# Performance work log

Measured on AMD Instinct MI355X. Metric: run time of the kernel, lower is better.

The kernel has to match this reference:

```python
import jax, jax.numpy as jnp
import numpy as np

WS = 4      # window_size
H = 128     # hidden_size
IN = 3      # input_size (1 control + 2 state channels)
OUT = 2     # out_size = input_size - 1


def _lstm_layer(x, Wih, Whh, b):
    # x: [B, S, Din] -> ys: [B, S, H], h/c: [B, H]. PyTorch gate order i,f,g,o.
    B = x.shape[0]
    xg = jnp.einsum('bsd,gd->bsg', x, Wih) + b  # precompute input projections

    def step(carry, xt):
        h, c = carry
        g = xt + h @ Whh.T
        i, f, gg, o = jnp.split(g, 4, axis=-1)
        c = jax.nn.sigmoid(f) * c + jax.nn.sigmoid(i) * jnp.tanh(gg)
        h = jax.nn.sigmoid(o) * jnp.tanh(c)
        return (h, c), h

    z = jnp.zeros((B, Whh.shape[1]), x.dtype)
    (h, c), ys = jax.lax.scan(step, (z, z), xg.transpose(1, 0, 2))
    return ys.transpose(1, 0, 2), h, c


def _lstm2(x, p):
    (Wih0, Whh0, b0), (Wih1, Whh1, b1) = p
    y0, h0, c0 = _lstm_layer(x, Wih0, Whh0, b0)
    y1, h1, c1 = _lstm_layer(y0, Wih1, Whh1, b1)
    return y1, jnp.stack([h0, h1]), jnp.stack([c0, c1])


def _forward(traj, Wih0, Whh0, bih0, bhh0, Wih1, Whh1, bih1, bhh1, Wl, bl):
    p = ((Wih0, Whh0, bih0 + bhh0), (Wih1, Whh1, bih1 + bhh1))
    head = lambda ys: ys[:, -1] @ Wl.T + bl  # linear applied to last LSTM step (== pred[:, -1])
    T = traj.shape[1]

    # initial window on raw trajectory
    ys, h, c = _lstm2(traj[:, :WS], p)
    out = traj[:, WS - 1:WS, 1:] + head(ys)[:, None, :]  # [B, 1, OUT]

    # warm-up phase: windows mix raw traj rows with predicted rows (features ordered [ctrl, out])
    for t in range(1, WS):
        tmp = jnp.concatenate([traj[:, WS + t:WS + t + 1, 0:1], out[:, t - 1:t, :]], axis=2)
        seq = jnp.concatenate([traj[:, t:WS + t - 1, :], tmp], axis=1)  # [B, WS, IN]
        ys, h, c = _lstm2(seq, p)
        out = jnp.concatenate([out, traj[:, WS + t - 1:WS + t, 1:] + head(ys)[:, None, :]], axis=1)

    nsteps = T - 2 * WS
    idx = WS + np.arange(nsteps)[:, None] + np.arange(WS)[None, :]  # [nsteps, WS]
    ctrl = traj[:, :, 0][:, idx].transpose(1, 0, 2)[..., None]      # [nsteps, B, WS, 1]

    def step(carry, ctrl_t):
        win, _, _ = carry
        seq = jnp.concatenate([win, ctrl_t], axis=2)  # [B, WS, OUT+1]
        ys, h, c = _lstm2(seq, p)
        new = win[:, -1, :] + head(ys)                # [B, OUT]
        win = jnp.concatenate([win[:, 1:], new[:, None, :]], axis=1)
        return (win, h, c), new

    (win, h, c), news = jax.lax.scan(step, (out, h, c), ctrl)
    out = jnp.concatenate([out, news.transpose(1, 0, 2)], axis=1)  # [B, T-WS, OUT]
    return out, h, c


def setup_inputs():
    key = jax.random.key(0)
    ks = jax.random.split(key, 11)
    B, T = 128, 256
    s = 1.0 / np.sqrt(H)
    u = lambda k, shp: jax.random.uniform(k, shp, jnp.float32, -s, s)
    return dict(
        one_full_traj=jax.random.normal(ks[0], (B, T, IN), jnp.float32),
        Wih0=u(ks[1], (4 * H, IN)), Whh0=u(ks[2], (4 * H, H)),
        bih0=u(ks[3], (4 * H,)), bhh0=u(ks[4], (4 * H,)),
        Wih1=u(ks[5], (4 * H, H)), Whh1=u(ks[6], (4 * H, H)),
        bih1=u(ks[7], (4 * H,)), bhh1=u(ks[8], (4 * H,)),
        Wl=u(ks[9], (OUT, H)), bl=u(ks[10], (OUT,)),
    )


def reference(one_full_traj, Wih0, Whh0, bih0, bhh0, Wih1, Whh1, bih1, bhh1, Wl, bl):
    # returns (out, h_n, c_n) matching torch's (out, hidden)
    return _forward(one_full_traj, Wih0, Whh0, bih0, bhh0, Wih1, Whh1, bih1, bhh1, Wl, bl)
```

## Files before the change

kernel.cpp:

```cpp
#include <hip/hip_runtime.h>

typedef _Float16 half2_t __attribute__((ext_vector_type(2)));
typedef unsigned int u32;

#define NW 252

__device__ inline u32 pk(float x, float y) {
  half2_t h; h.x = (_Float16)x; h.y = (_Float16)y;
  return __builtin_bit_cast(u32, h);
}

__device__ inline float fdot2(u32 a, u32 b, float c) {
#if __has_builtin(__builtin_amdgcn_fdot2)
  return __builtin_amdgcn_fdot2(__builtin_bit_cast(half2_t, a),
                                __builtin_bit_cast(half2_t, b), c, false);
#else
  half2_t ah = __builtin_bit_cast(half2_t, a);
  half2_t bh = __builtin_bit_cast(half2_t, b);
  return c + (float)ah.x * (float)bh.x + (float)ah.y * (float)bh.y;
#endif
}

__device__ inline float fast_rcp(float x) {
#if __has_builtin(__builtin_amdgcn_rcpf)
  return __builtin_amdgcn_rcpf(x);
#else
  return 1.0f / x;
#endif
}

__device__ inline float sigf(float x)  { return fast_rcp(1.0f + __expf(-x)); }
__device__ inline float tanh_(float x) { return 1.0f - 2.0f * fast_rcp(__expf(2.0f * x) + 1.0f); }

__device__ inline float quad_reduce(float v) {
  int x = __builtin_bit_cast(int, v);
  int y = __builtin_amdgcn_update_dpp(0, x, 0xB1, 0xF, 0xF, true);
  v += __builtin_bit_cast(float, y);
  x = __builtin_bit_cast(int, v);
  y = __builtin_amdgcn_update_dpp(0, x, 0x4E, 0xF, 0xF, true);
  v += __builtin_bit_cast(float, y);
  return v;
}

#define LOAD_SLICE(dst, basehalf)                                          \
  { const uint4* _p = (const uint4*)(basehalf) + ks * 4;                   \
    uint4 _q0 = _p[0], _q1 = _p[1], _q2 = _p[2], _q3 = _p[3];              \
    dst[0]=_q0.x;  dst[1]=_q0.y;  dst[2]=_q0.z;  dst[3]=_q0.w;             \
    dst[4]=_q1.x;  dst[5]=_q1.y;  dst[6]=_q1.z;  dst[7]=_q1.w;             \
    dst[8]=_q2.x;  dst[9]=_q2.y;  dst[10]=_q2.z; dst[11]=_q2.w;            \
    dst[12]=_q3.x; dst[13]=_q3.y; dst[14]=_q3.z; dst[15]=_q3.w; }

__global__ __launch_bounds__(512)
__attribute__((amdgpu_waves_per_eu(1, 2)))
void lstm_roll(
    const float* __restrict__ traj,
    const float* __restrict__ Wih0, const float* __restrict__ Whh0,
    const float* __restrict__ bih0, const float* __restrict__ bhh0,
    const float* __restrict__ Wih1, const float* __restrict__ Whh1,
    const float* __restrict__ bih1, const float* __restrict__ bhh1,
    const float* __restrict__ Wl,   const float* __restrict__ bl,
    float* __restrict__ out)
{
  const int b   = blockIdx.x;
  const int B   = gridDim.x;
  const int tid = threadIdx.x;
  const int j   = tid >> 2;
  const int ks  = tid & 3;

  __shared__ __align__(16) _Float16 h0buf[2][128];
  __shared__ __align__(16) _Float16 h1buf[2][128];
  __shared__ float sh_h1f[128];
  __shared__ float sh_Wl[256];
  __shared__ float trajS[256 * 3];
  __shared__ float preds[NW * 2];
  __shared__ __align__(16) float sh_w0b0[128 * 20];
  __shared__ __align__(16) float sh_b1[128 * 4];

  for (int i = tid; i < 768; i += 512) trajS[i] = traj[b * 768 + i];
  if (tid < 256) sh_Wl[tid] = Wl[tid];
  float blv = 0.0f;
  if (tid < 8) blv = bl[tid >> 2];
  {
    const int jj = tid >> 2, g = tid & 3;
    const int row = g * 128 + jj;
    sh_w0b0[jj * 20 + g * 4 + 0] = Wih0[row * 3 + 0];
    sh_w0b0[jj * 20 + g * 4 + 1] = Wih0[row * 3 + 1];
    sh_w0b0[jj * 20 + g * 4 + 2] = Wih0[row * 3 + 2];
    sh_w0b0[jj * 20 + g * 4 + 3] = bih0[row] + bhh0[row];
    sh_b1[jj * 4 + g] = bih1[row] + bhh1[row];
  }

  u32 wA[64], wB[64], wC[64];
#pragma unroll
  for (int g = 0; g < 4; ++g) {
    const int row = g * 128 + j;
    const float4* pA = (const float4*)(Whh0 + row * 128 + ks * 32);
    const float4* pB = (const float4*)(Wih1 + row * 128 + ks * 32);
    const float4* pC = (const float4*)(Whh1 + row * 128 + ks * 32);
#pragma unroll
    for (int q = 0; q < 8; ++q) {
      float4 fa = pA[q], fb = pB[q], fc = pC[q];
      wA[g*16 + q*2    ] = pk(fa.x, fa.y);
      wA[g*16 + q*2 + 1] = pk(fa.z, fa.w);
      wB[g*16 + q*2    ] = pk(fb.x, fb.y);
      wB[g*16 + q*2 + 1] = pk(fb.z, fb.w);
      wC[g*16 + q*2    ] = pk(fc.x, fc.y);
      wC[g*16 + q*2 + 1] = pk(fc.z, fc.w);
    }
  }

  float c0 = 0.f, c1 = 0.f, h0f = 0.f, h1f = 0.f;

  auto L0STEP = [&](int w_, int t_, int p_) {
    float acc0 = 0.f, acc1 = 0.f, acc2 = 0.f, acc3 = 0.f;
    if (ks == 0) {
      float x0, x1, x2;
      if (w_ < 4) {
        if (w_ == 0 || t_ < 3) {
          const float* r = &trajS[(w_ + t_) * 3];
          x0 = r[0]; x1 = r[1]; x2 = r[2];
        } else {
          x0 = trajS[(4 + w_) * 3];
          x1 = preds[(w_ - 1) * 2];
          x2 = preds[(w_ - 1) * 2 + 1];
        }
      } else {
        const int s_ = w_ - 4;
        x0 = preds[(s_ + t_) * 2];
        x1 = preds[(s_ + t_) * 2 + 1];
        x2 = trajS[(w_ + t_) * 3];
      }
      const float4* wb = (const float4*)&sh_w0b0[j * 20];
      float4 q0 = wb[0], q1 = wb[1], q2 = wb[2], q3 = wb[3];
      acc0 = q0.w + q0.x * x0 + q0.y * x1 + q0.z * x2;
      acc1 = q1.w + q1.x * x0 + q1.y * x1 + q1.z * x2;
      acc2 = q2.w + q2.x * x0 + q2.y * x1 + q2.z * x2;
      acc3 = q3.w + q3.x * x0 + q3.y * x1 + q3.z * x2;
    }
    if (t_ > 0) {
      u32 su[16];
      LOAD_SLICE(su, h0buf[p_]);
#pragma unroll
      for (int kk = 0; kk < 16; ++kk) {
        acc0 = fdot2(wA[     kk], su[kk], acc0);
        acc1 = fdot2(wA[16 + kk], su[kk], acc1);
        acc2 = fdot2(wA[32 + kk], su[kk], acc2);
        acc3 = fdot2(wA[48 + kk], su[kk], acc3);
      }
    }
    acc0 = quad_reduce(acc0); acc1 = quad_reduce(acc1);
    acc2 = quad_reduce(acc2); acc3 = quad_reduce(acc3);
    float ig = sigf(acc0), fg = sigf(acc1), gg = tanh_(acc2), og = sigf(acc3);
    float cp = t_ ? c0 : 0.f;
    c0  = fg * cp + ig * gg;
    h0f = og * tanh_(c0);
    if (ks == 0) h0buf[p_ ^ 1][j] = (_Float16)h0f;
  };

  auto L1STEP = [&](int t_, int p_) {
    float acc0 = 0.f, acc1 = 0.f, acc2 = 0.f, acc3 = 0.f;
    if (ks == 0) {
      float4 bb = *(const float4*)&sh_b1[j * 4];
      acc0 = bb.x; acc1 = bb.y; acc2 = bb.z; acc3 = bb.w;
    }
    {
      u32 sy[16];
      LOAD_SLICE(sy, h0buf[p_]);
#pragma unroll
      for (int kk = 0; kk < 16; ++kk) {
        acc0 = fdot2(wB[     kk], sy[kk], acc0);
        acc1 = fdot2(wB[16 + kk], sy[kk], acc1);
        acc2 = fdot2(wB[32 + kk], sy[kk], acc2);
        acc3 = fdot2(wB[48 + kk], sy[kk], acc3);
      }
    }
    if (t_ > 0) {
      u32 sh[16];
      LOAD_SLICE(sh, h1buf[p_]);
#pragma unroll
      for (int kk = 0; kk < 16; ++kk) {
        acc0 = fdot2(wC[     kk], sh[kk], acc0);
        acc1 = fdot2(wC[16 + kk], sh[kk], acc1);
        acc2 = fdot2(wC[32 + kk], sh[kk], acc2);
        acc3 = fdot2(wC[48 + kk], sh[kk], acc3);
      }
    }
    acc0 = quad_reduce(acc0); acc1 = quad_reduce(acc1);
    acc2 = quad_reduce(acc2); acc3 = quad_reduce(acc3);
    float ig = sigf(acc0), fg = sigf(acc1), gg = tanh_(acc2), og = sigf(acc3);
    float cp = t_ ? c1 : 0.f;
    c1  = fg * cp + ig * gg;
    h1f = og * tanh_(c1);
    if (ks == 0) {
      h1buf[p_ ^ 1][j] = (_Float16)h1f;
      if (t_ == 3) sh_h1f[j] = h1f;
    }
  };

  auto HD = [&](int w_) {
    if (tid < 8) {
      const int d = tid >> 2;
      const float* wrow = &sh_Wl[d * 128 + ks * 32];
      const float* hrow = &sh_h1f[ks * 32];
      float s = 0.f;
#pragma unroll
      for (int m = 0; m < 32; ++m) s = fmaf(wrow[m], hrow[m], s);
      s = quad_reduce(s);
      if (ks == 0) {
        float base = (w_ < 4) ? trajS[(3 + w_) * 3 + 1 + d] : preds[(w_ - 1) * 2 + d];
        preds[w_ * 2 + d] = base + s + blv;
      }
    }
  };

  __syncthreads();

  int p = 0;
  L0STEP(0, 0, p);
  __syncthreads(); p ^= 1;

#pragma unroll 1
  for (int w = 0; w < NW; ++w) {
    if (w > 0) HD(w - 1);
    L0STEP(w, 1, p);
    L1STEP(0, p);
    __syncthreads(); p ^= 1;
    L0STEP(w, 2, p);
    L1STEP(1, p);
    __syncthreads(); p ^= 1;
    L0STEP(w, 3, p);
    L1STEP(2, p);
    __syncthreads(); p ^= 1;
    L1STEP(3, p);
    if (w < NW - 1) L0STEP(w + 1, 0, p);
    __syncthreads(); p ^= 1;
  }

  HD(NW - 1);
  __syncthreads();

  for (int i = tid; i < NW * 2; i += 512) out[b * (NW * 2) + i] = preds[i];
  if (ks == 0) {
    const int oh = B * NW * 2;
    const int oc = oh + 2 * B * 128;
    out[oh +            b * 128 + j] = h0f;
    out[oh + B * 128 +  b * 128 + j] = h1f;
    out[oc +            b * 128 + j] = c0;
    out[oc + B * 128 +  b * 128 + j] = c1;
  }
}

extern "C" void kernel_launch(void* const* d_in, const int* in_sizes, int n_in,
                              void* d_out, int out_size, void* d_ws, size_t ws_size,
                              hipStream_t stream) {
  const float* traj = (const float*)d_in[0];
  const float* Wih0 = (const float*)d_in[1];
  const float* Whh0 = (const float*)d_in[2];
  const float* bih0 = (const float*)d_in[3];
  const float* bhh0 = (const float*)d_in[4];
  const float* Wih1 = (const float*)d_in[5];
  const float* Whh1 = (const float*)d_in[6];
  const float* bih1 = (const float*)d_in[7];
  const float* bhh1 = (const float*)d_in[8];
  const float* Wl   = (const float*)d_in[9];
  const float* bl   = (const float*)d_in[10];

  const int B = in_sizes[0] / (256 * 3);
  hipLaunchKernelGGL(lstm_roll, dim3(B), dim3(512), 0, stream,
                     traj, Wih0, Whh0, bih0, bhh0, Wih1, Whh1, bih1, bhh1,
                     Wl, bl, (float*)d_out);
}
```

Baseline: 1.379 ms.

## Split each hidden unit's dot products across 8 threads with 1024-thread blocks

Doubles the block to 1024 threads so each hidden unit is handled by 8 lanes instead of 4. Each lane keeps half as many packed fp16 weights in registers and does half the dot-product work per step. The partial sums are combined with a quad DPP reduce plus one xor shuffle. This shortens the serial per-step latency of the recurrent matvec, at the cost of an extra cross-lane reduction step, more waves contending at each barrier, and redundant gate math on the extra lanes.

```diff
diff --git a/kernel.cpp b/kernel.cpp
--- a/kernel.cpp
+++ b/kernel.cpp
@@ -41,17 +41,13 @@
   v += __builtin_bit_cast(float, y);
   return v;
 }
-
-#define LOAD_SLICE(dst, basehalf)                                          \
-  { const uint4* _p = (const uint4*)(basehalf) + ks * 4;                   \
-    uint4 _q0 = _p[0], _q1 = _p[1], _q2 = _p[2], _q3 = _p[3];              \
-    dst[0]=_q0.x;  dst[1]=_q0.y;  dst[2]=_q0.z;  dst[3]=_q0.w;             \
-    dst[4]=_q1.x;  dst[5]=_q1.y;  dst[6]=_q1.z;  dst[7]=_q1.w;             \
-    dst[8]=_q2.x;  dst[9]=_q2.y;  dst[10]=_q2.z; dst[11]=_q2.w;            \
-    dst[12]=_q3.x; dst[13]=_q3.y; dst[14]=_q3.z; dst[15]=_q3.w; }
-
-__global__ __launch_bounds__(512)
-__attribute__((amdgpu_waves_per_eu(1, 2)))
+__device__ inline float red8(float v) {
+  v = quad_reduce(v);
+  v += __shfl_xor(v, 4);
+  return v;
+}
+
+__global__ __launch_bounds__(1024)
 void lstm_roll(
     const float* __restrict__ traj,
     const float* __restrict__ Wih0, const float* __restrict__ Whh0,
@@ -64,8 +60,8 @@
   const int b   = blockIdx.x;
   const int B   = gridDim.x;
   const int tid = threadIdx.x;
-  const int j   = tid >> 2;
-  const int ks  = tid & 3;
+  const int j   = tid >> 3;
+  const int ks  = tid & 7;
 
   __shared__ __align__(16) _Float16 h0buf[2][128];
   __shared__ __align__(16) _Float16 h1buf[2][128];
@@ -76,11 +72,11 @@
   __shared__ __align__(16) float sh_w0b0[128 * 20];
   __shared__ __align__(16) float sh_b1[128 * 4];
 
-  for (int i = tid; i < 768; i += 512) trajS[i] = traj[b * 768 + i];
+  for (int i = tid; i < 768; i += 1024) trajS[i] = traj[b * 768 + i];
   if (tid < 256) sh_Wl[tid] = Wl[tid];
   float blv = 0.0f;
   if (tid < 8) blv = bl[tid >> 2];
-  {
+  if (tid < 512) {
     const int jj = tid >> 2, g = tid & 3;
     const int row = g * 128 + jj;
     sh_w0b0[jj * 20 + g * 4 + 0] = Wih0[row * 3 + 0];
@@ -90,22 +86,22 @@
     sh_b1[jj * 4 + g] = bih1[row] + bhh1[row];
   }
 
-  u32 wA[64], wB[64], wC[64];
+  u32 wA[32], wB[32], wC[32];
 #pragma unroll
   for (int g = 0; g < 4; ++g) {
     const int row = g * 128 + j;
-    const float4* pA = (const float4*)(Whh0 + row * 128 + ks * 32);
-    const float4* pB = (const float4*)(Wih1 + row * 128 + ks * 32);
-    const float4* pC = (const float4*)(Whh1 + row * 128 + ks * 32);
-#pragma unroll
-    for (int q = 0; q < 8; ++q) {
+    const float4* pA = (const float4*)(Whh0 + row * 128 + ks * 16);
+    const float4* pB = (const float4*)(Wih1 + row * 128 + ks * 16);
+    const float4* pC = (const float4*)(Whh1 + row * 128 + ks * 16);
+#pragma unroll
+    for (int q = 0; q < 4; ++q) {
       float4 fa = pA[q], fb = pB[q], fc = pC[q];
-      wA[g*16 + q*2    ] = pk(fa.x, fa.y);
-      wA[g*16 + q*2 + 1] = pk(fa.z, fa.w);
-      wB[g*16 + q*2    ] = pk(fb.x, fb.y);
-      wB[g*16 + q*2 + 1] = pk(fb.z, fb.w);
-      wC[g*16 + q*2    ] = pk(fc.x, fc.y);
-      wC[g*16 + q*2 + 1] = pk(fc.z, fc.w);
+      wA[g*8 + q*2    ] = pk(fa.x, fa.y);
+      wA[g*8 + q*2 + 1] = pk(fa.z, fa.w);
+      wB[g*8 + q*2    ] = pk(fb.x, fb.y);
+      wB[g*8 + q*2 + 1] = pk(fb.z, fb.w);
+      wC[g*8 + q*2    ] = pk(fc.x, fc.y);
+      wC[g*8 + q*2 + 1] = pk(fc.z, fc.w);
     }
   }
 
@@ -138,18 +134,19 @@
       acc3 = q3.w + q3.x * x0 + q3.y * x1 + q3.z * x2;
     }
     if (t_ > 0) {
-      u32 su[16];
-      LOAD_SLICE(su, h0buf[p_]);
-#pragma unroll
-      for (int kk = 0; kk < 16; ++kk) {
-        acc0 = fdot2(wA[     kk], su[kk], acc0);
-        acc1 = fdot2(wA[16 + kk], su[kk], acc1);
-        acc2 = fdot2(wA[32 + kk], su[kk], acc2);
-        acc3 = fdot2(wA[48 + kk], su[kk], acc3);
-      }
-    }
-    acc0 = quad_reduce(acc0); acc1 = quad_reduce(acc1);
-    acc2 = quad_reduce(acc2); acc3 = quad_reduce(acc3);
+      const uint4* _p = (const uint4*)(h0buf[p_]) + ks * 2;
+      uint4 q0 = _p[0], q1 = _p[1];
+      u32 s[8] = {q0.x, q0.y, q0.z, q0.w, q1.x, q1.y, q1.z, q1.w};
+#pragma unroll
+      for (int kk = 0; kk < 8; ++kk) {
+        acc0 = fdot2(wA[     kk], s[kk], acc0);
+        acc1 = fdot2(wA[ 8 + kk], s[kk], acc1);
+        acc2 = fdot2(wA[16 + kk], s[kk], acc2);
+        acc3 = fdot2(wA[24 + kk], s[kk], acc3);
+      }
+    }
+    acc0 = red8(acc0); acc1 = red8(acc1);
+    acc2 = red8(acc2); acc3 = red8(acc3);
     float ig = sigf(acc0), fg = sigf(acc1), gg = tanh_(acc2), og = sigf(acc3);
     float cp = t_ ? c0 : 0.f;
     c0  = fg * cp + ig * gg;
@@ -164,29 +161,31 @@
       acc0 = bb.x; acc1 = bb.y; acc2 = bb.z; acc3 = bb.w;
     }
     {
-      u32 sy[16];
-      LOAD_SLICE(sy, h0buf[p_]);
-#pragma unroll
-      for (int kk = 0; kk < 16; ++kk) {
-        acc0 = fdot2(wB[     kk], sy[kk], acc0);
-        acc1 = fdot2(wB[16 + kk], sy[kk], acc1);
-        acc2 = fdot2(wB[32 + kk], sy[kk], acc2);
-        acc3 = fdot2(wB[48 + kk], sy[kk], acc3);
+      const uint4* _p = (const uint4*)(h0buf[p_]) + ks * 2;
+      uint4 q0 = _p[0], q1 = _p[1];
+      u32 s[8] = {q0.x, q0.y, q0.z, q0.w, q1.x, q1.y, q1.z, q1.w};
+#pragma unroll
+      for (int kk = 0; kk < 8; ++kk) {
+        acc0 = fdot2(wB[     kk], s[kk], acc0);
+        acc1 = fdot2(wB[ 8 + kk], s[kk], acc1);
+        acc2 = fdot2(wB[16 + kk], s[kk], acc2);
+        acc3 = fdot2(wB[24 + kk], s[kk], acc3);
       }
     }
     if (t_ > 0) {
-      u32 sh[16];
-      LOAD_SLICE(sh, h1buf[p_]);
-#pragma unroll
-      for (int kk = 0; kk < 16; ++kk) {
-        acc0 = fdot2(wC[     kk], sh[kk], acc0);
-        acc1 = fdot2(wC[16 + kk], sh[kk], acc1);
-        acc2 = fdot2(wC[32 + kk], sh[kk], acc2);
-        acc3 = fdot2(wC[48 + kk], sh[kk], acc3);
-      }
-    }
-    acc0 = quad_reduce(acc0); acc1 = quad_reduce(acc1);
-    acc2 = quad_reduce(acc2); acc3 = quad_reduce(acc3);
+      const uint4* _p = (const uint4*)(h1buf[p_]) + ks * 2;
+      uint4 q0 = _p[0], q1 = _p[1];
+      u32 s[8] = {q0.x, q0.y, q0.z, q0.w, q1.x, q1.y, q1.z, q1.w};
+#pragma unroll
+      for (int kk = 0; kk < 8; ++kk) {
+        acc0 = fdot2(wC[     kk], s[kk], acc0);
+        acc1 = fdot2(wC[ 8 + kk], s[kk], acc1);
+        acc2 = fdot2(wC[16 + kk], s[kk], acc2);
+        acc3 = fdot2(wC[24 + kk], s[kk], acc3);
+      }
+    }
+    acc0 = red8(acc0); acc1 = red8(acc1);
+    acc2 = red8(acc2); acc3 = red8(acc3);
     float ig = sigf(acc0), fg = sigf(acc1), gg = tanh_(acc2), og = sigf(acc3);
     float cp = t_ ? c1 : 0.f;
     c1  = fg * cp + ig * gg;
@@ -200,13 +199,14 @@
   auto HD = [&](int w_) {
     if (tid < 8) {
       const int d = tid >> 2;
-      const float* wrow = &sh_Wl[d * 128 + ks * 32];
-      const float* hrow = &sh_h1f[ks * 32];
+      const int kq = tid & 3;
+      const float* wrow = &sh_Wl[d * 128 + kq * 32];
+      const float* hrow = &sh_h1f[kq * 32];
       float s = 0.f;
 #pragma unroll
       for (int m = 0; m < 32; ++m) s = fmaf(wrow[m], hrow[m], s);
       s = quad_reduce(s);
-      if (ks == 0) {
+      if (kq == 0) {
         float base = (w_ < 4) ? trajS[(3 + w_) * 3 + 1 + d] : preds[(w_ - 1) * 2 + d];
         preds[w_ * 2 + d] = base + s + blv;
       }
@@ -239,7 +239,7 @@
   HD(NW - 1);
   __syncthreads();
 
-  for (int i = tid; i < NW * 2; i += 512) out[b * (NW * 2) + i] = preds[i];
+  for (int i = tid; i < NW * 2; i += 1024) out[b * (NW * 2) + i] = preds[i];
   if (ks == 0) {
     const int oh = B * NW * 2;
     const int oc = oh + 2 * B * 128;
@@ -266,7 +266,7 @@
   const float* bl   = (const float*)d_in[10];
 
   const int B = in_sizes[0] / (256 * 3);
-  hipLaunchKernelGGL(lstm_roll, dim3(B), dim3(512), 0, stream,
+  hipLaunchKernelGGL(lstm_roll, dim3(B), dim3(1024), 0, stream,
                      traj, Wih0, Whh0, bih0, bhh0, Wih1, Whh1, bih1, bhh1,
                      Wl, bl, (float*)d_out);
 }
```

After: 2.054 ms. 48.9% more time.

## Pipeline four windows across timesteps to halve barriers per window

Applied to the files above, without the earlier changes.

Restructures the rollout so each iteration processes four overlapping windows at different timesteps (a wavefront over windows), keeping per-window h/c state in LDS slots instead of registers. Each window step now needs two barriers per iteration rather than four barriers per window with serialized layer steps. The head prediction is computed by a full-wave shuffle reduction and passed in registers to the next window's input. This adds four times the matvec work per iteration and more LDS traffic in exchange for fewer synchronization points and more independent work between barriers.

```diff
diff --git a/kernel.cpp b/kernel.cpp
--- a/kernel.cpp
+++ b/kernel.cpp
@@ -51,7 +51,7 @@
     dst[12]=_q3.x; dst[13]=_q3.y; dst[14]=_q3.z; dst[15]=_q3.w; }
 
 __global__ __launch_bounds__(512)
-__attribute__((amdgpu_waves_per_eu(1, 2)))
+__attribute__((amdgpu_num_vgpr(256)))
 void lstm_roll(
     const float* __restrict__ traj,
     const float* __restrict__ Wih0, const float* __restrict__ Whh0,
@@ -67,19 +67,20 @@
   const int j   = tid >> 2;
   const int ks  = tid & 3;
 
-  __shared__ __align__(16) _Float16 h0buf[2][128];
-  __shared__ __align__(16) _Float16 h1buf[2][128];
+  __shared__ __align__(16) _Float16 h0buf[4][2][128];
+  __shared__ __align__(16) _Float16 h1buf[4][2][128];
+  __shared__ float c0buf[4][128];
+  __shared__ float c1buf[4][128];
   __shared__ float sh_h1f[128];
   __shared__ float sh_Wl[256];
   __shared__ float trajS[256 * 3];
-  __shared__ float preds[NW * 2];
+  __shared__ float predsS[NW * 2];
   __shared__ __align__(16) float sh_w0b0[128 * 20];
   __shared__ __align__(16) float sh_b1[128 * 4];
 
   for (int i = tid; i < 768; i += 512) trajS[i] = traj[b * 768 + i];
   if (tid < 256) sh_Wl[tid] = Wl[tid];
-  float blv = 0.0f;
-  if (tid < 8) blv = bl[tid >> 2];
+  const float blv0 = bl[0], blv1 = bl[1];
   {
     const int jj = tid >> 2, g = tid & 3;
     const int row = g * 128 + jj;
@@ -109,144 +110,163 @@
     }
   }
 
-  float c0 = 0.f, c1 = 0.f, h0f = 0.f, h1f = 0.f;
-
-  auto L0STEP = [&](int w_, int t_, int p_) {
-    float acc0 = 0.f, acc1 = 0.f, acc2 = 0.f, acc3 = 0.f;
-    if (ks == 0) {
-      float x0, x1, x2;
-      if (w_ < 4) {
-        if (w_ == 0 || t_ < 3) {
-          const float* r = &trajS[(w_ + t_) * 3];
-          x0 = r[0]; x1 = r[1]; x2 = r[2];
+  float ppx = 0.f, ppy = 0.f;
+  float h0_last = 0.f, c0_last = 0.f, h1_last = 0.f, c1_last = 0.f;
+
+  __syncthreads();
+
+#pragma unroll 1
+  for (int k = -3; k < NW; ++k) {
+    const int wpar = k & 1;
+    const int rpar = wpar ^ 1;
+    float predx = 0.f, predy = 0.f;
+
+    if (k >= 1) {
+      const int l = tid & 63;
+      float h_a = sh_h1f[l], h_b = sh_h1f[64 + l];
+      float s0 = sh_Wl[      l] * h_a + sh_Wl[ 64 + l] * h_b;
+      float s1 = sh_Wl[128 + l] * h_a + sh_Wl[192 + l] * h_b;
+#pragma unroll
+      for (int off = 1; off < 64; off <<= 1) {
+        s0 += __shfl_xor(s0, off);
+        s1 += __shfl_xor(s1, off);
+      }
+      const int hw = k - 1;
+      const float basex = (hw < 4) ? trajS[(3 + hw) * 3 + 1] : ppx;
+      const float basey = (hw < 4) ? trajS[(3 + hw) * 3 + 2] : ppy;
+      predx = basex + s0 + blv0;
+      predy = basey + s1 + blv1;
+      if (tid == 0) { predsS[hw * 2] = predx; predsS[hw * 2 + 1] = predy; }
+    }
+
+#pragma unroll
+    for (int i = 0; i < 4; ++i) {
+      const int v = k + i;
+      if (v < 0 || v >= NW) continue;
+      const int t = 3 - i;
+      const int slot = v & 3;
+      float acc0 = 0.f, acc1 = 0.f, acc2 = 0.f, acc3 = 0.f;
+      if (ks == 0) {
+        float x0, x1, x2;
+        if (v < 4) {
+          if (v == 0 || t < 3) {
+            const float* r = &trajS[(v + t) * 3];
+            x0 = r[0]; x1 = r[1]; x2 = r[2];
+          } else {
+            x0 = trajS[(4 + v) * 3];
+            x1 = predx; x2 = predy;
+          }
         } else {
-          x0 = trajS[(4 + w_) * 3];
-          x1 = preds[(w_ - 1) * 2];
-          x2 = preds[(w_ - 1) * 2 + 1];
-        }
-      } else {
-        const int s_ = w_ - 4;
-        x0 = preds[(s_ + t_) * 2];
-        x1 = preds[(s_ + t_) * 2 + 1];
-        x2 = trajS[(w_ + t_) * 3];
-      }
-      const float4* wb = (const float4*)&sh_w0b0[j * 20];
-      float4 q0 = wb[0], q1 = wb[1], q2 = wb[2], q3 = wb[3];
-      acc0 = q0.w + q0.x * x0 + q0.y * x1 + q0.z * x2;
-      acc1 = q1.w + q1.x * x0 + q1.y * x1 + q1.z * x2;
-      acc2 = q2.w + q2.x * x0 + q2.y * x1 + q2.z * x2;
-      acc3 = q3.w + q3.x * x0 + q3.y * x1 + q3.z * x2;
-    }
-    if (t_ > 0) {
-      u32 su[16];
-      LOAD_SLICE(su, h0buf[p_]);
-#pragma unroll
-      for (int kk = 0; kk < 16; ++kk) {
-        acc0 = fdot2(wA[     kk], su[kk], acc0);
-        acc1 = fdot2(wA[16 + kk], su[kk], acc1);
-        acc2 = fdot2(wA[32 + kk], su[kk], acc2);
-        acc3 = fdot2(wA[48 + kk], su[kk], acc3);
-      }
-    }
-    acc0 = quad_reduce(acc0); acc1 = quad_reduce(acc1);
-    acc2 = quad_reduce(acc2); acc3 = quad_reduce(acc3);
-    float ig = sigf(acc0), fg = sigf(acc1), gg = tanh_(acc2), og = sigf(acc3);
-    float cp = t_ ? c0 : 0.f;
-    c0  = fg * cp + ig * gg;
-    h0f = og * tanh_(c0);
-    if (ks == 0) h0buf[p_ ^ 1][j] = (_Float16)h0f;
-  };
-
-  auto L1STEP = [&](int t_, int p_) {
-    float acc0 = 0.f, acc1 = 0.f, acc2 = 0.f, acc3 = 0.f;
-    if (ks == 0) {
-      float4 bb = *(const float4*)&sh_b1[j * 4];
-      acc0 = bb.x; acc1 = bb.y; acc2 = bb.z; acc3 = bb.w;
-    }
-    {
-      u32 sy[16];
-      LOAD_SLICE(sy, h0buf[p_]);
-#pragma unroll
-      for (int kk = 0; kk < 16; ++kk) {
-        acc0 = fdot2(wB[     kk], sy[kk], acc0);
-        acc1 = fdot2(wB[16 + kk], sy[kk], acc1);
-        acc2 = fdot2(wB[32 + kk], sy[kk], acc2);
-        acc3 = fdot2(wB[48 + kk], sy[kk], acc3);
-      }
-    }
-    if (t_ > 0) {
-      u32 sh[16];
-      LOAD_SLICE(sh, h1buf[p_]);
-#pragma unroll
-      for (int kk = 0; kk < 16; ++kk) {
-        acc0 = fdot2(wC[     kk], sh[kk], acc0);
-        acc1 = fdot2(wC[16 + kk], sh[kk], acc1);
-        acc2 = fdot2(wC[32 + kk], sh[kk], acc2);
-        acc3 = fdot2(wC[48 + kk], sh[kk], acc3);
-      }
-    }
-    acc0 = quad_reduce(acc0); acc1 = quad_reduce(acc1);
-    acc2 = quad_reduce(acc2); acc3 = quad_reduce(acc3);
-    float ig = sigf(acc0), fg = sigf(acc1), gg = tanh_(acc2), og = sigf(acc3);
-    float cp = t_ ? c1 : 0.f;
-    c1  = fg * cp + ig * gg;
-    h1f = og * tanh_(c1);
-    if (ks == 0) {
-      h1buf[p_ ^ 1][j] = (_Float16)h1f;
-      if (t_ == 3) sh_h1f[j] = h1f;
-    }
-  };
-
-  auto HD = [&](int w_) {
-    if (tid < 8) {
-      const int d = tid >> 2;
-      const float* wrow = &sh_Wl[d * 128 + ks * 32];
-      const float* hrow = &sh_h1f[ks * 32];
-      float s = 0.f;
-#pragma unroll
-      for (int m = 0; m < 32; ++m) s = fmaf(wrow[m], hrow[m], s);
-      s = quad_reduce(s);
-      if (ks == 0) {
-        float base = (w_ < 4) ? trajS[(3 + w_) * 3 + 1 + d] : preds[(w_ - 1) * 2 + d];
-        preds[w_ * 2 + d] = base + s + blv;
-      }
-    }
-  };
-
+          x0 = predx; x1 = predy;
+          x2 = trajS[(v + t) * 3];
+        }
+        const float4* wb = (const float4*)&sh_w0b0[j * 20];
+        float4 q0 = wb[0], q1 = wb[1], q2 = wb[2], q3 = wb[3];
+        acc0 = q0.w + q0.x * x0 + q0.y * x1 + q0.z * x2;
+        acc1 = q1.w + q1.x * x0 + q1.y * x1 + q1.z * x2;
+        acc2 = q2.w + q2.x * x0 + q2.y * x1 + q2.z * x2;
+        acc3 = q3.w + q3.x * x0 + q3.y * x1 + q3.z * x2;
+      }
+      if (t > 0) {
+        u32 s[16];
+        LOAD_SLICE(s, h0buf[slot][rpar]);
+#pragma unroll
+        for (int kk = 0; kk < 16; ++kk) {
+          acc0 = fdot2(wA[     kk], s[kk], acc0);
+          acc1 = fdot2(wA[16 + kk], s[kk], acc1);
+          acc2 = fdot2(wA[32 + kk], s[kk], acc2);
+          acc3 = fdot2(wA[48 + kk], s[kk], acc3);
+        }
+      }
+      acc0 = quad_reduce(acc0); acc1 = quad_reduce(acc1);
+      acc2 = quad_reduce(acc2); acc3 = quad_reduce(acc3);
+      if (ks == 0) {
+        float ig = sigf(acc0), fg = sigf(acc1), gg = tanh_(acc2), og = sigf(acc3);
+        float cp = t ? c0buf[slot][j] : 0.f;
+        float cn = fg * cp + ig * gg;
+        float hn = og * tanh_(cn);
+        c0buf[slot][j] = cn;
+        h0buf[slot][wpar][j] = (_Float16)hn;
+        if (v == NW - 1 && t == 3) { h0_last = hn; c0_last = cn; }
+      }
+    }
+    __syncthreads();
+
+#pragma unroll
+    for (int i = 0; i < 4; ++i) {
+      const int v = k + i;
+      if (v < 0 || v >= NW) continue;
+      const int t = 3 - i;
+      const int slot = v & 3;
+      float acc0 = 0.f, acc1 = 0.f, acc2 = 0.f, acc3 = 0.f;
+      if (ks == 0) {
+        float4 bb = *(const float4*)&sh_b1[j * 4];
+        acc0 = bb.x; acc1 = bb.y; acc2 = bb.z; acc3 = bb.w;
+      }
+      {
+        u32 s[16];
+        LOAD_SLICE(s, h0buf[slot][wpar]);
+#pragma unroll
+        for (int kk = 0; kk < 16; ++kk) {
+          acc0 = fdot2(wB[     kk], s[kk], acc0);
+          acc1 = fdot2(wB[16 + kk], s[kk], acc1);
+          acc2 = fdot2(wB[32 + kk], s[kk], acc2);
+          acc3 = fdot2(wB[48 + kk], s[kk], acc3);
+        }
+      }
+      if (t > 0) {
+        u32 s[16];
+        LOAD_SLICE(s, h1buf[slot][rpar]);
+#pragma unroll
+        for (int kk = 0; kk < 16; ++kk) {
+          acc0 = fdot2(wC[     kk], s[kk], acc0);
+          acc1 = fdot2(wC[16 + kk], s[kk], acc1);
+          acc2 = fdot2(wC[32 + kk], s[kk], acc2);
+          acc3 = fdot2(wC[48 + kk], s[kk], acc3);
+        }
+      }
+      acc0 = quad_reduce(acc0); acc1 = quad_reduce(acc1);
+      acc2 = quad_reduce(acc2); acc3 = quad_reduce(acc3);
+      if (ks == 0) {
+        float ig = sigf(acc0), fg = sigf(acc1), gg = tanh_(acc2), og = sigf(acc3);
+        float cp = t ? c1buf[slot][j] : 0.f;
+        float cn = fg * cp + ig * gg;
+        float hn = og * tanh_(cn);
+        c1buf[slot][j] = cn;
+        h1buf[slot][wpar][j] = (_Float16)hn;
+        if (t == 3) sh_h1f[j] = hn;
+        if (v == NW - 1 && t == 3) { h1_last = hn; c1_last = cn; }
+      }
+    }
+    ppx = predx; ppy = predy;
+    __syncthreads();
+  }
+
+  {
+    const int l = tid & 63;
+    float h_a = sh_h1f[l], h_b = sh_h1f[64 + l];
+    float s0 = sh_Wl[      l] * h_a + sh_Wl[ 64 + l] * h_b;
+    float s1 = sh_Wl[128 + l] * h_a + sh_Wl[192 + l] * h_b;
+#pragma unroll
+    for (int off = 1; off < 64; off <<= 1) {
+      s0 += __shfl_xor(s0, off);
+      s1 += __shfl_xor(s1, off);
+    }
+    if (tid == 0) {
+      predsS[(NW - 1) * 2    ] = ppx + s0 + blv0;
+      predsS[(NW - 1) * 2 + 1] = ppy + s1 + blv1;
+    }
+  }
   __syncthreads();
 
-  int p = 0;
-  L0STEP(0, 0, p);
-  __syncthreads(); p ^= 1;
-
-#pragma unroll 1
-  for (int w = 0; w < NW; ++w) {
-    if (w > 0) HD(w - 1);
-    L0STEP(w, 1, p);
-    L1STEP(0, p);
-    __syncthreads(); p ^= 1;
-    L0STEP(w, 2, p);
-    L1STEP(1, p);
-    __syncthreads(); p ^= 1;
-    L0STEP(w, 3, p);
-    L1STEP(2, p);
-    __syncthreads(); p ^= 1;
-    L1STEP(3, p);
-    if (w < NW - 1) L0STEP(w + 1, 0, p);
-    __syncthreads(); p ^= 1;
-  }
-
-  HD(NW - 1);
-  __syncthreads();
-
-  for (int i = tid; i < NW * 2; i += 512) out[b * (NW * 2) + i] = preds[i];
+  for (int i = tid; i < NW * 2; i += 512) out[b * (NW * 2) + i] = predsS[i];
   if (ks == 0) {
     const int oh = B * NW * 2;
     const int oc = oh + 2 * B * 128;
-    out[oh +            b * 128 + j] = h0f;
-    out[oh + B * 128 +  b * 128 + j] = h1f;
-    out[oc +            b * 128 + j] = c0;
-    out[oc + B * 128 +  b * 128 + j] = c1;
+    out[oh +            b * 128 + j] = h0_last;
+    out[oh + B * 128 +  b * 128 + j] = h1_last;
+    out[oc +            b * 128 + j] = c0_last;
+    out[oc + B * 128 +  b * 128 + j] = c1_last;
   }
 }
 
```

Measured after the change: 1.428 ms. 3.5% more time.
